# Optimization experiments

Hardware: AMD Instinct MI355X
Metric: run time of the kernel (lower is better)

## Reference

```python
import jax, jax.numpy as jnp
import numpy as np

RNN_DIMS = 1024
FC_DIMS = 1024
N_CLASSES = 256
BATCH = 128


def setup_inputs() -> dict:
    key = jax.random.key(0)
    ks = jax.random.split(key, 10)
    s = 1.0 / np.sqrt(RNN_DIMS)
    inp = {
        "x": jax.random.normal(ks[0], (BATCH, RNN_DIMS), dtype=jnp.float32),
        "h1": jax.random.normal(ks[1], (BATCH, RNN_DIMS), dtype=jnp.float32),
        # GRUCell params (PyTorch layout: [3*H, H] stacked as r,z,n)
        "w_ih": jax.random.uniform(ks[2], (3 * RNN_DIMS, RNN_DIMS), jnp.float32, -s, s),
        "w_hh": jax.random.uniform(ks[3], (3 * RNN_DIMS, RNN_DIMS), jnp.float32, -s, s),
        "b_ih": jax.random.uniform(ks[4], (3 * RNN_DIMS,), jnp.float32, -s, s),
        "b_hh": jax.random.uniform(ks[5], (3 * RNN_DIMS,), jnp.float32, -s, s),
        "w_fc1": jax.random.uniform(ks[6], (FC_DIMS, RNN_DIMS), jnp.float32, -s, s),
        "b_fc1": jax.random.uniform(ks[7], (FC_DIMS,), jnp.float32, -s, s),
        "w_fc3": jax.random.uniform(ks[8], (N_CLASSES, FC_DIMS), jnp.float32, -1.0 / np.sqrt(FC_DIMS), 1.0 / np.sqrt(FC_DIMS)),
        "b_fc3": jax.random.uniform(ks[9], (N_CLASSES,), jnp.float32, -1.0 / np.sqrt(FC_DIMS), 1.0 / np.sqrt(FC_DIMS)),
    }
    return inp


def reference(x, h1, w_ih, w_hh, b_ih, b_hh, w_fc1, b_fc1, w_fc3, b_fc3):
    # --- GRUCell (PyTorch semantics) ---
    gi = x @ w_ih.T + b_ih          # [B, 3H]
    gh = h1 @ w_hh.T + b_hh         # [B, 3H]
    i_r, i_z, i_n = jnp.split(gi, 3, axis=-1)
    h_r, h_z, h_n = jnp.split(gh, 3, axis=-1)
    r = jax.nn.sigmoid(i_r + h_r)
    z = jax.nn.sigmoid(i_z + h_z)
    n = jnp.tanh(i_n + r * h_n)
    h1_prime = (1.0 - z) * n + z * h1   # [B, H]
    # --- residual + MLP head ---
    res = h1_prime + x
    relu1 = jax.nn.relu(res @ w_fc1.T + b_fc1)   # [B, FC]
    out = relu1 @ w_fc3.T + b_fc3                # [B, N_CLASSES]
    return (out, h1_prime)
```

## Files before the change

kernel.cpp:

```cpp
#include <hip/hip_runtime.h>
#include <math.h>

typedef short bf16x8 __attribute__((ext_vector_type(8)));
typedef float f32x4 __attribute__((ext_vector_type(4)));

__device__ __forceinline__ int cvt2(float lo, float hi) {
    int r;
    asm("v_cvt_pk_bf16_f32 %0, %1, %2" : "=v"(r) : "v"(lo), "v"(hi));
    return r;
}

#define BAR() do {                                                        \
        asm volatile("s_waitcnt lgkmcnt(0)" ::: "memory");                \
        __builtin_amdgcn_s_barrier();                                     \
        __builtin_amdgcn_sched_barrier(0);                                \
    } while (0)

__global__ __launch_bounds__(256, 2) void gates_k(
    const float* __restrict__ x, const float* __restrict__ h1,
    const float* __restrict__ w_ih, const float* __restrict__ w_hh,
    const float* __restrict__ b_ih, const float* __restrict__ b_hh,
    float* __restrict__ h1p, float* __restrict__ res,
    float* __restrict__ zf1p, float* __restrict__ zout)
{
    __shared__ short As[2][128 * 64];
    __shared__ short Ws[2][96 * 64];
    const int tid  = threadIdx.x;
    const int lane = tid & 63;
    const int wv   = tid >> 6;

    {
        int id = blockIdx.x * 256 + tid;
        f32x4 z = {};
        *(f32x4*)(zf1p + id * 4) = z;
        zout[id] = 0.0f;
    }

    const int b    = blockIdx.x;
    const int tile = (b & 7) * 8 + ((b >> 3) >> 1);
    const int rg   = (b >> 3) & 1;
    const int c0   = tile * 16;
    const int row0 = rg * 64;

    const int r0 = tid >> 3, kc = tid & 7;

    const float* aP[4];
    int saI[4];
    #pragma unroll
    for (int i = 0; i < 4; ++i) {
        int ma = r0 + 32 * i;
        const float* src = (i < 2) ? x : h1;
        aP[i] = src + (row0 + (ma & 63)) * 1024 + kc * 8;
        saI[i] = (ma * 64 + kc * 8) ^ ((ma & 7) << 3);
    }
    const float* wP[3];
    int swI[3];
    #pragma unroll
    for (int i = 0; i < 3; ++i) {
        int mw = r0 + 32 * i;
        int g = mw >> 4;
        const float* src = (g < 3) ? w_ih : w_hh;
        wP[i] = src + ((g % 3) * 1024 + c0 + (mw & 15)) * 1024 + kc * 8;
        swI[i] = (mw * 64 + kc * 8) ^ ((mw & 7) << 3);
    }

    f32x4 A[2][4][2], W[2][3][2];
    f32x4 acc[6] = {};

#define G_ISSUE(kt, s) do {                                               \
        _Pragma("unroll")                                                 \
        for (int i = 0; i < 4; ++i) {                                     \
            A[s][i][0] = *(const f32x4*)(aP[i] + (kt) * 64);              \
            A[s][i][1] = *(const f32x4*)(aP[i] + (kt) * 64 + 4);          \
        }                                                                 \
        _Pragma("unroll")                                                 \
        for (int i = 0; i < 3; ++i) {                                     \
            W[s][i][0] = *(const f32x4*)(wP[i] + (kt) * 64);              \
            W[s][i][1] = *(const f32x4*)(wP[i] + (kt) * 64 + 4);          \
        }                                                                 \
    } while (0)

#define G_STAGE(s, bb) do {                                               \
        _Pragma("unroll")                                                 \
        for (int i = 0; i < 4; ++i) {                                     \
            int4 p;                                                       \
            p.x = cvt2(A[s][i][0][0], A[s][i][0][1]);                     \
            p.y = cvt2(A[s][i][0][2], A[s][i][0][3]);                     \
            p.z = cvt2(A[s][i][1][0], A[s][i][1][1]);                     \
            p.w = cvt2(A[s][i][1][2], A[s][i][1][3]);                     \
            *(int4*)&As[bb][saI[i]] = p;                                  \
        }                                                                 \
        _Pragma("unroll")                                                 \
        for (int i = 0; i < 3; ++i) {                                     \
            int4 q;                                                       \
            q.x = cvt2(W[s][i][0][0], W[s][i][0][1]);                     \
            q.y = cvt2(W[s][i][0][2], W[s][i][0][3]);                     \
            q.z = cvt2(W[s][i][1][0], W[s][i][1][1]);                     \
            q.w = cvt2(W[s][i][1][2], W[s][i][1][3]);                     \
            *(int4*)&Ws[bb][swI[i]] = q;                                  \
        }                                                                 \
    } while (0)

#define G_COMPUTE(bb) do {                                                \
        _Pragma("unroll")                                                 \
        for (int kk = 0; kk < 64; kk += 32) {                             \
            const int kw = kk + 8 * (lane >> 4);                          \
            const int ar = wv * 16 + (lane & 15);                         \
            bf16x8 afx = *(const bf16x8*)&As[bb][(ar * 64 + kw) ^ ((ar & 7) << 3)]; \
            bf16x8 afh = *(const bf16x8*)&As[bb][((ar + 64) * 64 + kw) ^ ((ar & 7) << 3)]; \
            _Pragma("unroll")                                             \
            for (int g = 0; g < 6; ++g) {                                 \
                int br = g * 16 + (lane & 15);                            \
                bf16x8 bw = *(const bf16x8*)&Ws[bb][(br * 64 + kw) ^ ((br & 7) << 3)]; \
                acc[g] = __builtin_amdgcn_mfma_f32_16x16x32_bf16(         \
                    (g < 3) ? afx : afh, bw, acc[g], 0, 0, 0);            \
            }                                                             \
        }                                                                 \
    } while (0)

    G_ISSUE(0, 0); G_ISSUE(1, 1);

    #pragma unroll 1
    for (int kt2 = 0; kt2 < 8; ++kt2) {
        const int kt = 2 * kt2;
        G_STAGE(0, 0); if (kt + 2 < 16) G_ISSUE(kt + 2, 0); BAR(); G_COMPUTE(0);
        G_STAGE(1, 1); if (kt + 3 < 16) G_ISSUE(kt + 3, 1); BAR(); G_COMPUTE(1);
    }

#undef G_ISSUE
#undef G_STAGE
#undef G_COMPUTE

    const int j = c0 + (lane & 15);
    const float bir = b_ih[j], biz = b_ih[1024 + j], bin = b_ih[2048 + j];
    const float bhr = b_hh[j], bhz = b_hh[1024 + j], bhn = b_hh[2048 + j];
    const int rbase = row0 + wv * 16 + (lane >> 4) * 4;
    #pragma unroll
    for (int r = 0; r < 4; ++r) {
        const int row = rbase + r;
        float ir  = acc[0][r] + bir, iz = acc[1][r] + biz, inn = acc[2][r] + bin;
        float hr  = acc[3][r] + bhr, hz = acc[4][r] + bhz, hn  = acc[5][r] + bhn;
        float rr = 1.0f / (1.0f + __expf(-(ir + hr)));
        float zz = 1.0f / (1.0f + __expf(-(iz + hz)));
        float nn = tanhf(inn + rr * hn);
        float h1v = h1[row * 1024 + j];
        float hp  = (1.0f - zz) * nn + zz * h1v;
        h1p[row * 1024 + j] = hp;
        res[row * 1024 + j] = hp + x[row * 1024 + j];
    }
}

template<int NT, bool ATOMIC, bool RELUA>
__global__ __launch_bounds__(256, 2) void gemm_k(
    const float* __restrict__ act, const float* __restrict__ wgt,
    const float* __restrict__ bias,
    float* __restrict__ out, int ldo, int nkt, int ksbits)
{
    constexpr int CT = NT / 16;
    __shared__ short As[2][64 * 64];
    __shared__ short Ws[2][NT * 64];

    const int tid  = threadIdx.x;
    const int lane = tid & 63;
    const int wv   = tid >> 6;

    const int ks   = blockIdx.x & ((1 << ksbits) - 1);
    const int rest = blockIdx.x >> ksbits;
    const int rg   = rest & 1;
    const int tile = rest >> 1;
    const int c0   = tile * NT;
    const int row0 = rg * 64;
    const int kt0  = ks * nkt;

    const int r0 = tid >> 3, kc = tid & 7;
    const float* aP = act + (row0 + r0) * 1024 + kt0 * 64 + kc * 8;
    const float* wP = wgt + (c0 + r0) * 1024 + kt0 * 64 + kc * 8;
    const bool wAct = (tid < NT * 8);

    const int saI0 = (r0 * 64 + kc * 8) ^ ((r0 & 7) << 3);
    const int saI1 = ((r0 + 32) * 64 + kc * 8) ^ ((r0 & 7) << 3);

    f32x4 A[4][4], W[4][2];
    f32x4 acc[CT] = {};

#define ISSUE(kt, s) do {                                                 \
        A[s][0] = *(const f32x4*)(aP + (kt) * 64);                        \
        A[s][1] = *(const f32x4*)(aP + (kt) * 64 + 4);                    \
        A[s][2] = *(const f32x4*)(aP + (kt) * 64 + 32768);                \
        A[s][3] = *(const f32x4*)(aP + (kt) * 64 + 32772);                \
        if (wAct) {                                                       \
            W[s][0] = *(const f32x4*)(wP + (kt) * 64);                    \
            W[s][1] = *(const f32x4*)(wP + (kt) * 64 + 4);                \
        }                                                                 \
    } while (0)

#define RL(v) (RELUA ? fmaxf((v), 0.0f) : (v))

#define STAGE(s, b) do {                                                  \
        int4 p0, p1;                                                      \
        p0.x = cvt2(RL(A[s][0][0]), RL(A[s][0][1]));                      \
        p0.y = cvt2(RL(A[s][0][2]), RL(A[s][0][3]));                      \
        p0.z = cvt2(RL(A[s][1][0]), RL(A[s][1][1]));                      \
        p0.w = cvt2(RL(A[s][1][2]), RL(A[s][1][3]));                      \
        p1.x = cvt2(RL(A[s][2][0]), RL(A[s][2][1]));                      \
        p1.y = cvt2(RL(A[s][2][2]), RL(A[s][2][3]));                      \
        p1.z = cvt2(RL(A[s][3][0]), RL(A[s][3][1]));                      \
        p1.w = cvt2(RL(A[s][3][2]), RL(A[s][3][3]));                      \
        *(int4*)&As[b][saI0] = p0;                                        \
        *(int4*)&As[b][saI1] = p1;                                        \
        if (wAct) {                                                       \
            int4 q;                                                       \
            q.x = cvt2(W[s][0][0], W[s][0][1]);                           \
            q.y = cvt2(W[s][0][2], W[s][0][3]);                           \
            q.z = cvt2(W[s][1][0], W[s][1][1]);                           \
            q.w = cvt2(W[s][1][2], W[s][1][3]);                           \
            *(int4*)&Ws[b][saI0] = q;                                     \
        }                                                                 \
    } while (0)

#define COMPUTE(b) do {                                                   \
        _Pragma("unroll")                                                 \
        for (int kk = 0; kk < 64; kk += 32) {                             \
            const int kw = kk + 8 * (lane >> 4);                          \
            const int ar = wv * 16 + (lane & 15);                         \
            bf16x8 af = *(const bf16x8*)&As[b][(ar * 64 + kw) ^ ((ar & 7) << 3)]; \
            bf16x8 bw[CT];                                                \
            _Pragma("unroll")                                             \
            for (int ct = 0; ct < CT; ++ct) {                             \
                int br = ct * 16 + (lane & 15);                           \
                bw[ct] = *(const bf16x8*)&Ws[b][(br * 64 + kw) ^ ((br & 7) << 3)]; \
            }                                                             \
            _Pragma("unroll")                                             \
            for (int ct = 0; ct < CT; ++ct)                               \
                acc[ct] = __builtin_amdgcn_mfma_f32_16x16x32_bf16(        \
                    af, bw[ct], acc[ct], 0, 0, 0);                        \
        }                                                                 \
    } while (0)

    ISSUE(0, 0); ISSUE(1, 1); ISSUE(2, 2); ISSUE(3, 3);

    #pragma unroll 1
    for (int g = 0; g < nkt / 4; ++g) {
        const int kt = 4 * g;
        STAGE(0, 0); if (kt + 4 < nkt) ISSUE(kt + 4, 0); BAR(); COMPUTE(0);
        STAGE(1, 1); if (kt + 5 < nkt) ISSUE(kt + 5, 1); BAR(); COMPUTE(1);
        STAGE(2, 0); if (kt + 6 < nkt) ISSUE(kt + 6, 2); BAR(); COMPUTE(0);
        STAGE(3, 1); if (kt + 7 < nkt) ISSUE(kt + 7, 3); BAR(); COMPUTE(1);
    }

#undef ISSUE
#undef RL
#undef STAGE
#undef COMPUTE

    #pragma unroll
    for (int ct = 0; ct < CT; ++ct) {
        int col = c0 + ct * 16 + (lane & 15);
        float bv = (bias && ks == 0) ? bias[col] : 0.0f;
        #pragma unroll
        for (int r = 0; r < 4; ++r) {
            int row = row0 + wv * 16 + (lane >> 4) * 4 + r;
            float v = acc[ct][r] + bv;
            if (ATOMIC) unsafeAtomicAdd(&out[row * ldo + col], v);
            else        out[row * ldo + col] = v;
        }
    }
}

extern "C" void kernel_launch(void* const* d_in, const int* in_sizes, int n_in,
                              void* d_out, int out_size, void* d_ws, size_t ws_size,
                              hipStream_t stream)
{
    const float* x     = (const float*)d_in[0];
    const float* h1    = (const float*)d_in[1];
    const float* w_ih  = (const float*)d_in[2];
    const float* w_hh  = (const float*)d_in[3];
    const float* b_ih  = (const float*)d_in[4];
    const float* b_hh  = (const float*)d_in[5];
    const float* w_fc1 = (const float*)d_in[6];
    const float* b_fc1 = (const float*)d_in[7];
    const float* w_fc3 = (const float*)d_in[8];
    const float* b_fc3 = (const float*)d_in[9];

    float* out = (float*)d_out;
    float* h1p = out + 128 * 256;

    float* ws  = (float*)d_ws;
    float* res = ws;
    float* f1p = ws + 128 * 1024;

    gates_k<<<128, 256, 0, stream>>>(x, h1, w_ih, w_hh, b_ih, b_hh,
                                     h1p, res, f1p, out);
    gemm_k<16, true, false><<<256, 256, 0, stream>>>(
        res, w_fc1, b_fc1, f1p, 1024, 8, 1);
    gemm_k<16, true, true><<<64, 256, 0, stream>>>(
        f1p, w_fc3, b_fc3, out, 256, 8, 1);
}
```

Baseline: 30.20 us.

## Halve gate tile rows, split waves by gate half, deepen split-K in FC GEMMs

```diff
diff --git a/kernel.cpp b/kernel.cpp
--- a/kernel.cpp
+++ b/kernel.cpp
@@ -23,36 +23,26 @@
     float* __restrict__ h1p, float* __restrict__ res,
     float* __restrict__ zf1p, float* __restrict__ zout)
 {
-    __shared__ short As[2][128 * 64];
+    __shared__ short As[2][64 * 64];
     __shared__ short Ws[2][96 * 64];
     const int tid  = threadIdx.x;
     const int lane = tid & 63;
     const int wv   = tid >> 6;
-
-    {
-        int id = blockIdx.x * 256 + tid;
-        f32x4 z = {};
-        *(f32x4*)(zf1p + id * 4) = z;
-        zout[id] = 0.0f;
-    }
-
     const int b    = blockIdx.x;
-    const int tile = (b & 7) * 8 + ((b >> 3) >> 1);
-    const int rg   = (b >> 3) & 1;
+
+    if (tid < 128) { f32x4 z = {}; *(f32x4*)(zf1p + b * 512 + tid * 4) = z; }
+    if (tid < 32)  { f32x4 z = {}; *(f32x4*)(zout + b * 128 + tid * 4) = z; }
+
+    const int tile = b & 63;
+    const int rgq  = b >> 6;
     const int c0   = tile * 16;
-    const int row0 = rg * 64;
-
+    const int row0 = rgq * 32;
     const int r0 = tid >> 3, kc = tid & 7;
 
-    const float* aP[4];
-    int saI[4];
-    #pragma unroll
-    for (int i = 0; i < 4; ++i) {
-        int ma = r0 + 32 * i;
-        const float* src = (i < 2) ? x : h1;
-        aP[i] = src + (row0 + (ma & 63)) * 1024 + kc * 8;
-        saI[i] = (ma * 64 + kc * 8) ^ ((ma & 7) << 3);
-    }
+    const float* aP[2] = { x  + (row0 + r0) * 1024 + kc * 8,
+                           h1 + (row0 + r0) * 1024 + kc * 8 };
+    const int saI[2] = { (r0 * 64 + kc * 8) ^ ((r0 & 7) << 3),
+                         ((r0 + 32) * 64 + kc * 8) ^ ((r0 & 7) << 3) };
     const float* wP[3];
     int swI[3];
     #pragma unroll
@@ -64,12 +54,16 @@
         swI[i] = (mw * 64 + kc * 8) ^ ((mw & 7) << 3);
     }
 
-    f32x4 A[2][4][2], W[2][3][2];
-    f32x4 acc[6] = {};
+    f32x4 A[2][2][2], W[2][3][2];
+    f32x4 acc[3] = {};
+
+    const int rowg = wv & 1;
+    const int hsel = wv >> 1;
+    const int gbase = hsel * 3;
 
 #define G_ISSUE(kt, s) do {                                               \
         _Pragma("unroll")                                                 \
-        for (int i = 0; i < 4; ++i) {                                     \
+        for (int i = 0; i < 2; ++i) {                                     \
             A[s][i][0] = *(const f32x4*)(aP[i] + (kt) * 64);              \
             A[s][i][1] = *(const f32x4*)(aP[i] + (kt) * 64 + 4);          \
         }                                                                 \
@@ -82,7 +76,7 @@
 
 #define G_STAGE(s, bb) do {                                               \
         _Pragma("unroll")                                                 \
-        for (int i = 0; i < 4; ++i) {                                     \
+        for (int i = 0; i < 2; ++i) {                                     \
             int4 p;                                                       \
             p.x = cvt2(A[s][i][0][0], A[s][i][0][1]);                     \
             p.y = cvt2(A[s][i][0][2], A[s][i][0][3]);                     \
@@ -105,48 +99,58 @@
         _Pragma("unroll")                                                 \
         for (int kk = 0; kk < 64; kk += 32) {                             \
             const int kw = kk + 8 * (lane >> 4);                          \
-            const int ar = wv * 16 + (lane & 15);                         \
-            bf16x8 afx = *(const bf16x8*)&As[bb][(ar * 64 + kw) ^ ((ar & 7) << 3)]; \
-            bf16x8 afh = *(const bf16x8*)&As[bb][((ar + 64) * 64 + kw) ^ ((ar & 7) << 3)]; \
+            const int ma = hsel * 32 + rowg * 16 + (lane & 15);           \
+            bf16x8 af = *(const bf16x8*)&As[bb][(ma * 64 + kw) ^ ((ma & 7) << 3)]; \
             _Pragma("unroll")                                             \
-            for (int g = 0; g < 6; ++g) {                                 \
-                int br = g * 16 + (lane & 15);                            \
+            for (int gg = 0; gg < 3; ++gg) {                              \
+                int br = (gbase + gg) * 16 + (lane & 15);                 \
                 bf16x8 bw = *(const bf16x8*)&Ws[bb][(br * 64 + kw) ^ ((br & 7) << 3)]; \
-                acc[g] = __builtin_amdgcn_mfma_f32_16x16x32_bf16(         \
-                    (g < 3) ? afx : afh, bw, acc[g], 0, 0, 0);            \
+                acc[gg] = __builtin_amdgcn_mfma_f32_16x16x32_bf16(        \
+                    af, bw, acc[gg], 0, 0, 0);                            \
             }                                                             \
         }                                                                 \
     } while (0)
 
     G_ISSUE(0, 0); G_ISSUE(1, 1);
-
     #pragma unroll 1
     for (int kt2 = 0; kt2 < 8; ++kt2) {
         const int kt = 2 * kt2;
         G_STAGE(0, 0); if (kt + 2 < 16) G_ISSUE(kt + 2, 0); BAR(); G_COMPUTE(0);
         G_STAGE(1, 1); if (kt + 3 < 16) G_ISSUE(kt + 3, 1); BAR(); G_COMPUTE(1);
     }
-
 #undef G_ISSUE
 #undef G_STAGE
 #undef G_COMPUTE
 
-    const int j = c0 + (lane & 15);
-    const float bir = b_ih[j], biz = b_ih[1024 + j], bin = b_ih[2048 + j];
-    const float bhr = b_hh[j], bhz = b_hh[1024 + j], bhn = b_hh[2048 + j];
-    const int rbase = row0 + wv * 16 + (lane >> 4) * 4;
-    #pragma unroll
-    for (int r = 0; r < 4; ++r) {
-        const int row = rbase + r;
-        float ir  = acc[0][r] + bir, iz = acc[1][r] + biz, inn = acc[2][r] + bin;
-        float hr  = acc[3][r] + bhr, hz = acc[4][r] + bhz, hn  = acc[5][r] + bhn;
-        float rr = 1.0f / (1.0f + __expf(-(ir + hr)));
-        float zz = 1.0f / (1.0f + __expf(-(iz + hz)));
-        float nn = tanhf(inn + rr * hn);
-        float h1v = h1[row * 1024 + j];
-        float hp  = (1.0f - zz) * nn + zz * h1v;
-        h1p[row * 1024 + j] = hp;
-        res[row * 1024 + j] = hp + x[row * 1024 + j];
+    float* xch = (float*)&As[0][0];
+    if (hsel) {
+        #pragma unroll
+        for (int gg = 0; gg < 3; ++gg)
+            #pragma unroll
+            for (int r = 0; r < 4; ++r)
+                xch[(rowg * 3 + gg) * 256 + ((lane >> 4) * 4 + r) * 16 + (lane & 15)]
+                    = acc[gg][r];
+    }
+    BAR();
+    if (!hsel) {
+        const int j = c0 + (lane & 15);
+        const float bir = b_ih[j], biz = b_ih[1024 + j], bin = b_ih[2048 + j];
+        const float bhr = b_hh[j], bhz = b_hh[1024 + j], bhn = b_hh[2048 + j];
+        const int rbase = row0 + rowg * 16 + (lane >> 4) * 4;
+        #pragma unroll
+        for (int r = 0; r < 4; ++r) {
+            const int row = rbase + r;
+            const int xb  = rowg * 3 * 256 + ((lane >> 4) * 4 + r) * 16 + (lane & 15);
+            float ir  = acc[0][r] + bir, iz = acc[1][r] + biz, inn = acc[2][r] + bin;
+            float hr  = xch[xb] + bhr, hz = xch[xb + 256] + bhz, hn = xch[xb + 512] + bhn;
+            float rr = 1.0f / (1.0f + __expf(-(ir + hr)));
+            float zz = 1.0f / (1.0f + __expf(-(iz + hz)));
+            float nn = tanhf(inn + rr * hn);
+            float h1v = h1[row * 1024 + j];
+            float hp  = (1.0f - zz) * nn + zz * h1v;
+            h1p[row * 1024 + j] = hp;
+            res[row * 1024 + j] = hp + x[row * 1024 + j];
+        }
     }
 }
 
@@ -289,10 +293,10 @@
     float* res = ws;
     float* f1p = ws + 128 * 1024;
 
-    gates_k<<<128, 256, 0, stream>>>(x, h1, w_ih, w_hh, b_ih, b_hh,
+    gates_k<<<256, 256, 0, stream>>>(x, h1, w_ih, w_hh, b_ih, b_hh,
                                      h1p, res, f1p, out);
-    gemm_k<16, true, false><<<256, 256, 0, stream>>>(
-        res, w_fc1, b_fc1, f1p, 1024, 8, 1);
-    gemm_k<16, true, true><<<64, 256, 0, stream>>>(
-        f1p, w_fc3, b_fc3, out, 256, 8, 1);
+    gemm_k<16, true, false><<<512, 256, 0, stream>>>(
+        res, w_fc1, b_fc1, f1p, 1024, 4, 2);
+    gemm_k<16, true, true><<<128, 256, 0, stream>>>(
+        f1p, w_fc3, b_fc3, out, 256, 4, 2);
 }
```

Measured after the change: 25.45 us (median of 3 runs). 1.19x faster.
